# Performance work log

Measured on AMD Instinct MI355X. Metric: run time of the kernel, lower is better.

Reference implementation:

```python
import jax, jax.numpy as jnp
import numpy as np

N_DRUG, N_PROT = 20000, 8000
D_DRUG, D_PROT = 300, 1280
HIDDEN, OUT = 512, 5
N_EDGE, N_LBL = 500000, 200000


def setup_inputs() -> dict:
    key = jax.random.key(0)
    ks = jax.random.split(key, 12)
    inp = {
        "x_drug": jax.random.normal(ks[0], (N_DRUG, D_DRUG), dtype=jnp.float32),
        "x_prot": jax.random.normal(ks[1], (N_PROT, D_PROT), dtype=jnp.float32),
        "edge_src": jax.random.randint(ks[2], (N_EDGE,), 0, N_DRUG, dtype=jnp.int32),
        "edge_dst": jax.random.randint(ks[3], (N_EDGE,), 0, N_PROT, dtype=jnp.int32),
        "lbl_src": jax.random.randint(ks[4], (N_LBL,), 0, N_DRUG, dtype=jnp.int32),
        "lbl_dst": jax.random.randint(ks[5], (N_LBL,), 0, N_PROT, dtype=jnp.int32),
        # SAGEConv params: lin_l (on aggregated src msgs, with bias), lin_r (on dst, no bias)
        "W_l": jax.random.normal(ks[6], (HIDDEN, D_DRUG), dtype=jnp.float32) / np.sqrt(D_DRUG),
        "b_l": jnp.zeros((HIDDEN,), dtype=jnp.float32),
        "W_r": jax.random.normal(ks[7], (HIDDEN, D_PROT), dtype=jnp.float32) / np.sqrt(D_PROT),
        # final edge classifier Linear(D_DRUG + HIDDEN, OUT)
        "W_lin": jax.random.normal(ks[8], (OUT, D_DRUG + HIDDEN), dtype=jnp.float32) / np.sqrt(D_DRUG + HIDDEN),
        "b_lin": jnp.zeros((OUT,), dtype=jnp.float32),
    }
    return inp


def reference(x_drug, x_prot, edge_src, edge_dst, lbl_src, lbl_dst,
              W_l, b_l, W_r, W_lin, b_lin):
    # --- bipartite SAGEConv((drug, protein)) with default mean aggregation ---
    msg = x_drug[edge_src]                                   # [E, D_DRUG] gather
    agg = jax.ops.segment_sum(msg, edge_dst, num_segments=N_PROT)   # [N_PROT, D_DRUG]
    cnt = jax.ops.segment_sum(jnp.ones((edge_dst.shape[0],), jnp.float32),
                              edge_dst, num_segments=N_PROT)
    mean = agg / jnp.clip(cnt, 1.0, None)[:, None]           # mean over in-neighbors
    prot_emb_all = mean @ W_l.T + b_l + x_prot @ W_r.T       # [N_PROT, HIDDEN]

    # --- gather endpoints for labeled edges, concat, linear ---
    drug_emb = x_drug[lbl_src]                               # [L, D_DRUG]
    prot_emb = prot_emb_all[lbl_dst]                         # [L, HIDDEN]
    edge_emb = jnp.concatenate([drug_emb, prot_emb], axis=1) # [L, D_DRUG+HIDDEN]
    return edge_emb @ W_lin.T + b_lin                        # [L, OUT]
```

## Files before the change

kernel.cpp:

```cpp
#include <hip/hip_runtime.h>

#define N_DRUG 20000
#define N_PROT 8000
#define D_DRUG 300
#define D_PROT 1280
#define HIDDEN 512
#define OUT_D  5
#define N_EDGE 500000
#define N_LBL  200000
#define WLD    812
#define CAP    128
#define OVF_MAX 65536

__global__ void k_stage1(const float* __restrict__ W_l, const float* __restrict__ W_r,
                         const float* __restrict__ W_lin, const float* __restrict__ b_l,
                         const int* __restrict__ edge_src, const int* __restrict__ edge_dst,
                         float* __restrict__ A, float* __restrict__ B, float* __restrict__ c,
                         int* __restrict__ cnt, int* __restrict__ novf,
                         int* __restrict__ bucket, int* __restrict__ ovf) {
    int b = blockIdx.x;
    if (b < 248) {
        int t  = (b % 31) * 256 + threadIdx.x;
        int h0 = (b / 31) * 64;
        const int nA = OUT_D * D_DRUG;
        const int nB = OUT_D * D_PROT;
        if (t < nA) {
            int o = t / D_DRUG, k = t - o * D_DRUG;
            const float* wp = W_lin + o * WLD + D_DRUG + h0;
            const float* wl = W_l + (size_t)h0 * D_DRUG + k;
            float s = 0.f;
#pragma unroll 4
            for (int h = 0; h < 64; ++h) s += wp[h] * wl[h * D_DRUG];
            atomicAdd(&A[t], s);
        } else if (t < nA + nB) {
            int u = t - nA;
            int o = u / D_PROT, k = u - o * D_PROT;
            const float* wp = W_lin + o * WLD + D_DRUG + h0;
            const float* wr = W_r + (size_t)h0 * D_PROT + k;
            float s = 0.f;
#pragma unroll 4
            for (int h = 0; h < 64; ++h) s += wp[h] * wr[h * D_PROT];
            atomicAdd(&B[u], s);
        } else if (t < nA + nB + OUT_D) {
            int o = t - nA - nB;
            const float* wp = W_lin + o * WLD + D_DRUG + h0;
            float s = 0.f;
            for (int h = 0; h < 64; ++h) s += wp[h] * b_l[h0 + h];
            atomicAdd(&c[o], s);
        }
    } else {
        int base = (b - 248) * 2048 + threadIdx.x;
#pragma unroll
        for (int i = 0; i < 8; ++i) {
            int e = base + i * 256;
            if (e < N_EDGE) {
                int s = edge_src[e], d = edge_dst[e];
                int r = atomicAdd(&cnt[d], 1);
                if (r < CAP) {
                    bucket[d * CAP + r] = s;
                } else {
                    int o = atomicAdd(novf, 1);
                    if (o < OVF_MAX) { ovf[2 * o] = d; ovf[2 * o + 1] = s; }
                }
            }
        }
    }
}

__global__ void k_stage2(const float* __restrict__ x_drug, const float* __restrict__ x_prot,
                         const float* __restrict__ A, const float* __restrict__ B,
                         const float* __restrict__ c, const float* __restrict__ W_lin,
                         float* __restrict__ P_A, float* __restrict__ drugO,
                         float* __restrict__ protO) {
    int b = blockIdx.x;
    if (b < 1250) {
        int gid = b * 256 + threadIdx.x;
        int row = gid >> 4;
        int sub = threadIdx.x & 15;
        const float4* xr = (const float4*)(x_drug + (size_t)row * D_DRUG);
        float acc[10];
#pragma unroll
        for (int i = 0; i < 10; ++i) acc[i] = 0.f;
        for (int k = sub; k < D_DRUG / 4; k += 16) {
            float4 x = xr[k];
#pragma unroll
            for (int o = 0; o < OUT_D; ++o) {
                float4 a = ((const float4*)(A + o * D_DRUG))[k];
                acc[o] += x.x * a.x + x.y * a.y + x.z * a.z + x.w * a.w;
                float4 w = ((const float4*)(W_lin + o * WLD))[k];
                acc[5 + o] += x.x * w.x + x.y * w.y + x.z * w.z + x.w * w.w;
            }
        }
#pragma unroll
        for (int i = 0; i < 10; ++i) {
            float v = acc[i];
            for (int m = 8; m; m >>= 1) v += __shfl_xor(v, m, 64);
            acc[i] = v;
        }
        if (sub < OUT_D) {
            P_A[row * OUT_D + sub]   = acc[sub];
            drugO[row * OUT_D + sub] = acc[5 + sub];
        }
    } else {
        int wave = ((b - 1250) * 256 + threadIdx.x) >> 6;
        int lane = threadIdx.x & 63;
        const float4* xr = (const float4*)(x_prot + (size_t)wave * D_PROT);
        float acc[OUT_D] = {0.f, 0.f, 0.f, 0.f, 0.f};
        for (int k = lane; k < D_PROT / 4; k += 64) {
            float4 x = xr[k];
#pragma unroll
            for (int o = 0; o < OUT_D; ++o) {
                float4 bb = ((const float4*)(B + o * D_PROT))[k];
                acc[o] += x.x * bb.x + x.y * bb.y + x.z * bb.z + x.w * bb.w;
            }
        }
#pragma unroll
        for (int o = 0; o < OUT_D; ++o) {
            float v = acc[o];
            for (int off = 32; off; off >>= 1) v += __shfl_xor(v, off, 64);
            acc[o] = v;
        }
        if (lane < OUT_D) protO[wave * OUT_D + lane] = acc[lane] + c[lane];
    }
}

__global__ void k_gather(const int* __restrict__ cnt, const int* __restrict__ novf,
                         const int* __restrict__ bucket, const int* __restrict__ ovf,
                         const float* __restrict__ P_A, float* __restrict__ protO) {
    int wave = (blockIdx.x * blockDim.x + threadIdx.x) >> 6;
    int lane = threadIdx.x & 63;
    if (wave >= N_PROT) return;
    int deg = cnt[wave];
    int m = deg < CAP ? deg : CAP;
    float acc[OUT_D] = {0.f, 0.f, 0.f, 0.f, 0.f};
    const int* br = &bucket[wave * CAP];
    for (int j = lane; j < m; j += 64) {
        const float* p = &P_A[br[j] * OUT_D];
#pragma unroll
        for (int o = 0; o < OUT_D; ++o) acc[o] += p[o];
    }
    if (deg > CAP) {
        int nv = *novf; if (nv > OVF_MAX) nv = OVF_MAX;
        for (int j = lane; j < nv; j += 64) {
            if (ovf[2 * j] == wave) {
                const float* p = &P_A[ovf[2 * j + 1] * OUT_D];
#pragma unroll
                for (int o = 0; o < OUT_D; ++o) acc[o] += p[o];
            }
        }
    }
#pragma unroll
    for (int o = 0; o < OUT_D; ++o) {
        float v = acc[o];
        for (int off = 32; off; off >>= 1) v += __shfl_xor(v, off, 64);
        acc[o] = v;
    }
    if (lane < OUT_D)
        protO[wave * OUT_D + lane] += acc[lane] / fmaxf((float)deg, 1.f);
}

__global__ void k_final(const int* __restrict__ lbl_src, const int* __restrict__ lbl_dst,
                        const float* __restrict__ drugO, const float* __restrict__ protO,
                        const float* __restrict__ b_lin, float* __restrict__ out) {
    int l = blockIdx.x * blockDim.x + threadIdx.x;
    if (l >= N_LBL) return;
    int s = lbl_src[l], d = lbl_dst[l];
    const float* dr = &drugO[s * OUT_D];
    const float* pr = &protO[d * OUT_D];
    float* op = &out[(size_t)l * OUT_D];
    op[0] = dr[0] + pr[0] + b_lin[0];
    op[1] = dr[1] + pr[1] + b_lin[1];
    op[2] = dr[2] + pr[2] + b_lin[2];
    op[3] = dr[3] + pr[3] + b_lin[3];
    op[4] = dr[4] + pr[4] + b_lin[4];
}

extern "C" void kernel_launch(void* const* d_in, const int* in_sizes, int n_in,
                              void* d_out, int out_size, void* d_ws, size_t ws_size,
                              hipStream_t stream) {
    const float* x_drug   = (const float*)d_in[0];
    const float* x_prot   = (const float*)d_in[1];
    const int*   edge_src = (const int*)d_in[2];
    const int*   edge_dst = (const int*)d_in[3];
    const int*   lbl_src  = (const int*)d_in[4];
    const int*   lbl_dst  = (const int*)d_in[5];
    const float* W_l      = (const float*)d_in[6];
    const float* b_l      = (const float*)d_in[7];
    const float* W_r      = (const float*)d_in[8];
    const float* W_lin    = (const float*)d_in[9];
    const float* b_lin    = (const float*)d_in[10];
    float* out = (float*)d_out;

    char* ws = (char*)d_ws;
    int*   cnt    = (int*)  (ws + 0);
    int*   novf   = (int*)  (ws + 32000);
    float* A      = (float*)(ws + 32016);
    float* B      = (float*)(ws + 38016);
    float* c      = (float*)(ws + 63616);
    float* P_A    = (float*)(ws + 64000);
    float* drugO  = (float*)(ws + 464000);
    float* protO  = (float*)(ws + 864000);
    int*   bucket = (int*)  (ws + 1024000);
    int*   ovf    = (int*)  (ws + 5120000);

    hipMemsetAsync(ws, 0, 63648, stream);
    k_stage1<<<493, 256, 0, stream>>>(W_l, W_r, W_lin, b_l, edge_src, edge_dst,
                                      A, B, c, cnt, novf, bucket, ovf);
    k_stage2<<<3250, 256, 0, stream>>>(x_drug, x_prot, A, B, c, W_lin,
                                       P_A, drugO, protO);
    k_gather<<<(N_PROT * 64) / 256, 256, 0, stream>>>(cnt, novf, bucket, ovf, P_A, protO);
    k_final<<<(N_LBL + 255) / 256, 256, 0, stream>>>(lbl_src, lbl_dst, drugO, protO, b_lin, out);
}
```

Before: 165.0 us.

## Move edge bucketing into the projection kernel to overlap with GEMV work

Splits the weight-folding step into its own small kernel. The edge bucketing (atomic counting and scatter into per-protein buckets) now runs inside the second kernel, alongside the drug and protein projection blocks, using 128 grid-stride blocks. This lets the latency-bound atomic scatter overlap with the bandwidth-bound x_drug/x_prot reads, where before it sat on the critical path of the first kernel. The cost is fewer blocks doing the scatter, each with longer loops, which could make it the tail.

```diff
diff --git a/kernel.cpp b/kernel.cpp
--- a/kernel.cpp
+++ b/kernel.cpp
@@ -11,72 +11,65 @@
 #define WLD    812
 #define CAP    128
 #define OVF_MAX 65536
-
-__global__ void k_stage1(const float* __restrict__ W_l, const float* __restrict__ W_r,
-                         const float* __restrict__ W_lin, const float* __restrict__ b_l,
-                         const int* __restrict__ edge_src, const int* __restrict__ edge_dst,
-                         float* __restrict__ A, float* __restrict__ B, float* __restrict__ c,
-                         int* __restrict__ cnt, int* __restrict__ novf,
-                         int* __restrict__ bucket, int* __restrict__ ovf) {
+#define SBLK   128
+
+__global__ void k_fold(const float* __restrict__ W_l, const float* __restrict__ W_r,
+                       const float* __restrict__ W_lin, const float* __restrict__ b_l,
+                       float* __restrict__ A, float* __restrict__ B, float* __restrict__ c) {
+    int t  = (blockIdx.x % 31) * 256 + threadIdx.x;
+    int h0 = (blockIdx.x / 31) * 64;
+    const int nA = OUT_D * D_DRUG;
+    const int nB = OUT_D * D_PROT;
+    if (t < nA) {
+        int o = t / D_DRUG, k = t - o * D_DRUG;
+        const float* wp = W_lin + o * WLD + D_DRUG + h0;
+        const float* wl = W_l + (size_t)h0 * D_DRUG + k;
+        float s = 0.f;
+#pragma unroll 4
+        for (int h = 0; h < 64; ++h) s += wp[h] * wl[h * D_DRUG];
+        atomicAdd(&A[t], s);
+    } else if (t < nA + nB) {
+        int u = t - nA;
+        int o = u / D_PROT, k = u - o * D_PROT;
+        const float* wp = W_lin + o * WLD + D_DRUG + h0;
+        const float* wr = W_r + (size_t)h0 * D_PROT + k;
+        float s = 0.f;
+#pragma unroll 4
+        for (int h = 0; h < 64; ++h) s += wp[h] * wr[h * D_PROT];
+        atomicAdd(&B[u], s);
+    } else if (t < nA + nB + OUT_D) {
+        int o = t - nA - nB;
+        const float* wp = W_lin + o * WLD + D_DRUG + h0;
+        float s = 0.f;
+        for (int h = 0; h < 64; ++h) s += wp[h] * b_l[h0 + h];
+        atomicAdd(&c[o], s);
+    }
+}
+
+__global__ void k_mid(const float* __restrict__ x_drug, const float* __restrict__ x_prot,
+                      const int* __restrict__ edge_src, const int* __restrict__ edge_dst,
+                      const float* __restrict__ A, const float* __restrict__ B,
+                      const float* __restrict__ c, const float* __restrict__ W_lin,
+                      int* __restrict__ cnt, int* __restrict__ novf,
+                      int* __restrict__ bucket, int* __restrict__ ovf,
+                      float* __restrict__ P_A, float* __restrict__ drugO,
+                      float* __restrict__ protO) {
     int b = blockIdx.x;
-    if (b < 248) {
-        int t  = (b % 31) * 256 + threadIdx.x;
-        int h0 = (b / 31) * 64;
-        const int nA = OUT_D * D_DRUG;
-        const int nB = OUT_D * D_PROT;
-        if (t < nA) {
-            int o = t / D_DRUG, k = t - o * D_DRUG;
-            const float* wp = W_lin + o * WLD + D_DRUG + h0;
-            const float* wl = W_l + (size_t)h0 * D_DRUG + k;
-            float s = 0.f;
-#pragma unroll 4
-            for (int h = 0; h < 64; ++h) s += wp[h] * wl[h * D_DRUG];
-            atomicAdd(&A[t], s);
-        } else if (t < nA + nB) {
-            int u = t - nA;
-            int o = u / D_PROT, k = u - o * D_PROT;
-            const float* wp = W_lin + o * WLD + D_DRUG + h0;
-            const float* wr = W_r + (size_t)h0 * D_PROT + k;
-            float s = 0.f;
-#pragma unroll 4
-            for (int h = 0; h < 64; ++h) s += wp[h] * wr[h * D_PROT];
-            atomicAdd(&B[u], s);
-        } else if (t < nA + nB + OUT_D) {
-            int o = t - nA - nB;
-            const float* wp = W_lin + o * WLD + D_DRUG + h0;
-            float s = 0.f;
-            for (int h = 0; h < 64; ++h) s += wp[h] * b_l[h0 + h];
-            atomicAdd(&c[o], s);
-        }
-    } else {
-        int base = (b - 248) * 2048 + threadIdx.x;
-#pragma unroll
-        for (int i = 0; i < 8; ++i) {
-            int e = base + i * 256;
-            if (e < N_EDGE) {
-                int s = edge_src[e], d = edge_dst[e];
-                int r = atomicAdd(&cnt[d], 1);
-                if (r < CAP) {
-                    bucket[d * CAP + r] = s;
-                } else {
-                    int o = atomicAdd(novf, 1);
-                    if (o < OVF_MAX) { ovf[2 * o] = d; ovf[2 * o + 1] = s; }
-                }
-            }
-        }
-    }
-}
-
-__global__ void k_stage2(const float* __restrict__ x_drug, const float* __restrict__ x_prot,
-                         const float* __restrict__ A, const float* __restrict__ B,
-                         const float* __restrict__ c, const float* __restrict__ W_lin,
-                         float* __restrict__ P_A, float* __restrict__ drugO,
-                         float* __restrict__ protO) {
-    int b = blockIdx.x;
-    if (b < 1250) {
-        int gid = b * 256 + threadIdx.x;
-        int row = gid >> 4;
-        int sub = threadIdx.x & 15;
+    int tid = threadIdx.x;
+    if (b < SBLK) {
+        for (int e = b * 256 + tid; e < N_EDGE; e += SBLK * 256) {
+            int s = edge_src[e], d = edge_dst[e];
+            int r = atomicAdd(&cnt[d], 1);
+            if (r < CAP) {
+                bucket[d * CAP + r] = s;
+            } else {
+                int o = atomicAdd(novf, 1);
+                if (o < OVF_MAX) { ovf[2 * o] = d; ovf[2 * o + 1] = s; }
+            }
+        }
+    } else if (b < SBLK + 1250) {
+        int row = (b - SBLK) * 16 + (tid >> 4);
+        int sub = tid & 15;
         const float4* xr = (const float4*)(x_drug + (size_t)row * D_DRUG);
         float acc[10];
 #pragma unroll
@@ -102,9 +95,9 @@
             drugO[row * OUT_D + sub] = acc[5 + sub];
         }
     } else {
-        int wave = ((b - 1250) * 256 + threadIdx.x) >> 6;
-        int lane = threadIdx.x & 63;
-        const float4* xr = (const float4*)(x_prot + (size_t)wave * D_PROT);
+        int row  = (b - SBLK - 1250) * 4 + (tid >> 6);
+        int lane = tid & 63;
+        const float4* xr = (const float4*)(x_prot + (size_t)row * D_PROT);
         float acc[OUT_D] = {0.f, 0.f, 0.f, 0.f, 0.f};
         for (int k = lane; k < D_PROT / 4; k += 64) {
             float4 x = xr[k];
@@ -120,7 +113,7 @@
             for (int off = 32; off; off >>= 1) v += __shfl_xor(v, off, 64);
             acc[o] = v;
         }
-        if (lane < OUT_D) protO[wave * OUT_D + lane] = acc[lane] + c[lane];
+        if (lane < OUT_D) protO[row * OUT_D + lane] = acc[lane] + c[lane];
     }
 }
 
@@ -204,10 +197,10 @@
     int*   ovf    = (int*)  (ws + 5120000);
 
     hipMemsetAsync(ws, 0, 63648, stream);
-    k_stage1<<<493, 256, 0, stream>>>(W_l, W_r, W_lin, b_l, edge_src, edge_dst,
-                                      A, B, c, cnt, novf, bucket, ovf);
-    k_stage2<<<3250, 256, 0, stream>>>(x_drug, x_prot, A, B, c, W_lin,
-                                       P_A, drugO, protO);
+    k_fold<<<248, 256, 0, stream>>>(W_l, W_r, W_lin, b_l, A, B, c);
+    k_mid<<<SBLK + 1250 + 2000, 256, 0, stream>>>(
+        x_drug, x_prot, edge_src, edge_dst, A, B, c, W_lin,
+        cnt, novf, bucket, ovf, P_A, drugO, protO);
     k_gather<<<(N_PROT * 64) / 256, 256, 0, stream>>>(cnt, novf, bucket, ovf, P_A, protO);
     k_final<<<(N_LBL + 255) / 256, 256, 0, stream>>>(lbl_src, lbl_dst, drugO, protO, b_lin, out);
 }
```

Measured after the change: 169.3 us. 1.03x slower.
